# Optimization experiments

Hardware: AMD Instinct MI355X
Metric: run time of the kernel (lower is better)

The kernel has to match this reference:

```python
import jax, jax.numpy as jnp
import numpy as np

NUM_HEADS = 12
SCRA_SCALING = 10.0
EPS = 1e-12  # F.normalize default eps


def setup_inputs() -> dict:
    key = jax.random.key(0)
    ks = jax.random.split(key, 5)
    B, N, C = 2, 2048, 768
    return {
        "x": jax.random.normal(ks[0], (B, N, C), dtype=jnp.float32),
        "qkv_w": jax.random.normal(ks[1], (3 * C, C), dtype=jnp.float32) * 0.02,
        "qkv_b": jax.random.normal(ks[2], (3 * C,), dtype=jnp.float32) * 0.02,
        "proj_w": jax.random.normal(ks[3], (C, C), dtype=jnp.float32) * 0.02,
        "proj_b": jax.random.normal(ks[4], (C,), dtype=jnp.float32) * 0.02,
    }


def reference(x, qkv_w, qkv_b, proj_w, proj_b):
    B, N, C = x.shape
    H = NUM_HEADS
    D = C // H
    scale = D ** -0.5

    xt = jnp.transpose(x, (1, 0, 2))  # [N, B, C]
    qkv = xt @ qkv_w.T + qkv_b        # [N, B, 3C]
    q, k, v = jnp.split(qkv, 3, axis=-1)

    def to_bh(t):  # [N, B, C] -> [B*H, N, D]
        return jnp.transpose(t.reshape(N, B * H, D), (1, 0, 2))

    q, k, v = to_bh(q), to_bh(k), to_bh(v)

    # Stage 1: standard attention
    attn = jax.nn.softmax(jnp.einsum('bnd,bmd->bnm', q, k) * scale, axis=-1)
    out = jnp.einsum('bnm,bmd->bnd', attn, v)  # [B*H, N, D]
    out = jnp.transpose(out, (1, 0, 2)).reshape(N, B, C)
    out = out @ proj_w.T + proj_b              # first proj
    out = jnp.transpose(out.reshape(N, B * H, D), (1, 0, 2))  # [B*H, N, D]

    # Stage 2: self-correlation attention with data-dependent masking
    norm = jnp.linalg.norm(out, axis=-1, keepdims=True)
    sim_tokens = out / jnp.maximum(norm, EPS)
    sim = jnp.einsum('bnd,bmd->bnm', sim_tokens, sim_tokens) * SCRA_SCALING
    sim = jnp.where(sim < 0, -jnp.inf, sim)
    sim = jax.nn.softmax(sim, axis=-1)
    out2 = jnp.einsum('bnm,bmd->bnd', sim, v)
    out2 = jnp.transpose(out2, (1, 0, 2)).reshape(N, B, C)
    out2 = out2 @ proj_w.T + proj_b            # second proj (same weights)

    return jnp.transpose(out2, (1, 0, 2))      # [B, N, C]
```

## Files before the change

### kernel.cpp

```cpp
#include <hip/hip_runtime.h>

typedef unsigned short u16;
typedef __bf16 bf16_t;
typedef bf16_t bf16x8 __attribute__((ext_vector_type(8)));
typedef float f32x4 __attribute__((ext_vector_type(4)));

static __device__ __forceinline__ u16 f2bf(float f) {
  unsigned u = __builtin_bit_cast(unsigned, f);
  u += 0x7FFFu + ((u >> 16) & 1u);
  return (u16)(u >> 16);
}
static __device__ __forceinline__ bf16x8 ldfrag(const u16* p) {
  return __builtin_bit_cast(bf16x8, *(const uint4*)p);
}
static __device__ __forceinline__ float fexp2(float x) {
#if __has_builtin(__builtin_amdgcn_exp2f)
  return __builtin_amdgcn_exp2f(x);
#else
  return __expf(x * 0.69314718056f);
#endif
}
static __device__ __forceinline__ unsigned pack_hi16(unsigned hi, unsigned lo) {
#if __has_builtin(__builtin_amdgcn_perm)
  return __builtin_amdgcn_perm(hi, lo, 0x07060302u);
#else
  return (lo >> 16) | (hi & 0xFFFF0000u);
#endif
}
static __device__ __forceinline__ uint4 pack8_rtz(float4 a, float4 b) {
  uint4 o;
  o.x = pack_hi16(__builtin_bit_cast(unsigned, a.y), __builtin_bit_cast(unsigned, a.x));
  o.y = pack_hi16(__builtin_bit_cast(unsigned, a.w), __builtin_bit_cast(unsigned, a.z));
  o.z = pack_hi16(__builtin_bit_cast(unsigned, b.y), __builtin_bit_cast(unsigned, b.x));
  o.w = pack_hi16(__builtin_bit_cast(unsigned, b.w), __builtin_bit_cast(unsigned, b.z));
  return o;
}
static __device__ __forceinline__ int sw(int row, int chunk) {
  return (row << 6) + ((chunk ^ (row & 7)) << 3);
}

#define QWSZ 1769472
#define PWSZ 589824

__global__ __launch_bounds__(256) void convert_w(
    const float* __restrict__ qw, const float* __restrict__ pw,
    u16* __restrict__ qwb, u16* __restrict__ pwb)
{
  const int i = (blockIdx.x * 256 + threadIdx.x) * 8;
  const float* src; u16* dst; int off;
  if (i < QWSZ) { src = qw; dst = qwb; off = i; }
  else { src = pw; dst = pwb; off = i - QWSZ; }
  float4 a = *(const float4*)(src + off), b = *(const float4*)(src + off + 4);
  u16 t[8] = {f2bf(a.x), f2bf(a.y), f2bf(a.z), f2bf(a.w),
              f2bf(b.x), f2bf(b.y), f2bf(b.z), f2bf(b.w)};
  *(uint4*)(dst + off) = *(const uint4*)t;
}

template<int MODE>
__global__ __launch_bounds__(256, MODE == 0 ? 2 : 3) void gemm_nt(
    const void* __restrict__ Araw, const u16* __restrict__ W,
    const float* __restrict__ bias,
    u16* __restrict__ d0, u16* __restrict__ d1, u16* __restrict__ d2,
    float* __restrict__ df)
{
  constexpr int BM = (MODE == 0) ? 128 : 64;
  constexpr int MI = (MODE == 0) ? 4 : 2;
  constexpr int AP = BM / 32;
  __shared__ __align__(16) u16 sA[2][BM * 64];
  __shared__ __align__(16) u16 sB[2][128 * 64];
  const float* Af = (const float*)Araw;
  const u16*   Ab = (const u16*)Araw;
  const int tid = threadIdx.x;
  const int m0 = blockIdx.y * BM, n0 = blockIdx.x * 128;
  const int w = tid >> 6, lane = tid & 63, l16 = lane & 15, quad = lane >> 4;
  const int wm = (w >> 1) * (BM / 2), wn = (w & 1) * 64;

  f32x4 acc[MI][4] = {};
  const int sr = tid >> 3, ch = tid & 7, sc = ch * 8;

  #pragma unroll
  for (int p = 0; p < AP; p++) {
    const int row = sr + p * 32;
    if (MODE == 0) {
      const float* ap = Af + (size_t)(m0 + row) * 768 + sc;
      *(uint4*)(sA[0] + sw(row, ch)) =
          pack8_rtz(*(const float4*)ap, *(const float4*)(ap + 4));
    } else {
      *(uint4*)(sA[0] + sw(row, ch)) =
          *(const uint4*)(Ab + (size_t)(m0 + row) * 768 + sc);
    }
  }
  #pragma unroll
  for (int p = 0; p < 4; p++) {
    const int row = sr + p * 32;
    *(uint4*)(sB[0] + sw(row, ch)) = *(const uint4*)(W + (size_t)(n0 + row) * 768 + sc);
  }
  __syncthreads();

  for (int kt = 0; kt < 12; kt++) {
    const int buf = kt & 1;
    const bool pre = (kt + 1 < 12);
    float4 ra0[AP], ra1[AP];
    uint4 rab[AP], rb[4];
    if (pre) {
      const int kc = (kt + 1) * 64 + sc;
      #pragma unroll
      for (int p = 0; p < AP; p++) {
        if (MODE == 0) {
          const float* ap = Af + (size_t)(m0 + sr + p * 32) * 768 + kc;
          ra0[p] = *(const float4*)ap;
          ra1[p] = *(const float4*)(ap + 4);
        } else {
          rab[p] = *(const uint4*)(Ab + (size_t)(m0 + sr + p * 32) * 768 + kc);
        }
      }
      #pragma unroll
      for (int p = 0; p < 4; p++)
        rb[p] = *(const uint4*)(W + (size_t)(n0 + sr + p * 32) * 768 + kc);
    }
    #pragma unroll
    for (int ks = 0; ks < 2; ks++) {
      bf16x8 af[MI], bfv[4];
      #pragma unroll
      for (int i = 0; i < MI; i++)
        af[i] = ldfrag(sA[buf] + sw(wm + i * 16 + l16, ks * 4 + quad));
      #pragma unroll
      for (int i = 0; i < 4; i++)
        bfv[i] = ldfrag(sB[buf] + sw(wn + i * 16 + l16, ks * 4 + quad));
      #pragma unroll
      for (int mi = 0; mi < MI; mi++)
        #pragma unroll
        for (int ni = 0; ni < 4; ni++)
          acc[mi][ni] = __builtin_amdgcn_mfma_f32_16x16x32_bf16(af[mi], bfv[ni], acc[mi][ni], 0, 0, 0);
    }
    if (pre) {
      #pragma unroll
      for (int p = 0; p < AP; p++) {
        if (MODE == 0)
          *(uint4*)(sA[buf ^ 1] + sw(sr + p * 32, ch)) = pack8_rtz(ra0[p], ra1[p]);
        else
          *(uint4*)(sA[buf ^ 1] + sw(sr + p * 32, ch)) = rab[p];
      }
      #pragma unroll
      for (int p = 0; p < 4; p++)
        *(uint4*)(sB[buf ^ 1] + sw(sr + p * 32, ch)) = rb[p];
    }
    __syncthreads();
  }

  if (MODE == 0) {
    #pragma unroll
    for (int ni = 0; ni < 4; ni++) {
      const int gn = n0 + wn + ni * 16 + l16;
      const float bv = bias[gn];
      const int which = gn / 768;
      const int c = gn - which * 768, hh = c >> 6, d = c & 63;
      #pragma unroll
      for (int mi = 0; mi < 4; mi++) {
        const int gm0 = m0 + wm + mi * 16 + quad * 4;
        const int bb = gm0 >> 11, nt0 = gm0 & 2047;
        if (which == 2) {
          u16 t[4];
          #pragma unroll
          for (int r = 0; r < 4; r++) t[r] = f2bf(acc[mi][ni][r] + bv);
          *(uint2*)(d2 + (((size_t)(bb * 12 + hh)) * 64 + d) * 2048 + nt0) =
              *(const uint2*)t;
        } else {
          u16* dst = (which == 0) ? d0 : d1;
          #pragma unroll
          for (int r = 0; r < 4; r++)
            dst[(((size_t)(bb * 12 + hh)) * 2048 + nt0 + r) * 64 + d] =
                f2bf(acc[mi][ni][r] + bv);
        }
      }
    }
  } else if (MODE == 1) {
    #pragma unroll
    for (int mi = 0; mi < MI; mi++) {
      #pragma unroll
      for (int r = 0; r < 4; r++) {
        float v[4]; float ss = 0.f;
        #pragma unroll
        for (int ni = 0; ni < 4; ni++) {
          v[ni] = acc[mi][ni][r] + bias[n0 + wn + ni * 16 + l16];
          ss += v[ni] * v[ni];
        }
        #pragma unroll
        for (int off = 1; off < 16; off <<= 1) ss += __shfl_xor(ss, off);
        const float scl = 1.f / fmaxf(sqrtf(ss), 1e-12f);
        const int gm = m0 + wm + mi * 16 + quad * 4 + r;
        const int nt = gm >> 1, b = gm & 1;
        #pragma unroll
        for (int ni = 0; ni < 4; ni++) {
          const int gn = n0 + wn + ni * 16 + l16, h = gn >> 6, d = gn & 63;
          d0[(((size_t)(b * 12 + h)) * 2048 + nt) * 64 + d] = f2bf(v[ni] * scl);
        }
      }
    }
  } else {
    #pragma unroll
    for (int ni = 0; ni < 4; ni++) {
      const int gn = n0 + wn + ni * 16 + l16;
      const float bv = bias[gn];
      #pragma unroll
      for (int mi = 0; mi < MI; mi++) {
        #pragma unroll
        for (int r = 0; r < 4; r++) {
          const int gm = m0 + wm + mi * 16 + quad * 4 + r;
          const int nt = gm >> 1, b = gm & 1;
          df[((size_t)b * 2048 + nt) * 768 + gn] = acc[mi][ni][r] + bv;
        }
      }
    }
  }
}

template<int MODE>
__global__ __launch_bounds__(256, 2) void flash_attn(
    const u16* __restrict__ Qm, const u16* __restrict__ Km,
    const u16* __restrict__ VT,
    float* __restrict__ partN, float* __restrict__ partL)
{
  constexpr int N = 2048;
  __shared__ __align__(16) u16 sU[128 * 64];
  __shared__ __align__(16) u16 sK[2][64 * 64];
  __shared__ __align__(16) u16 sVT[2][64 * 64];
  const int tid = threadIdx.x;
  const int bh = blockIdx.y;
  const int qt = blockIdx.x >> 1, half = blockIdx.x & 1;
  const int m0 = qt * 128, j0 = half * 1024;
  const int w = tid >> 6, lane = tid & 63, l16 = lane & 15, quad = lane >> 4;

  constexpr float SC = (MODE == 1) ? 0.18033688011112042f
                                   : 14.426950408889634f;
  constexpr float M0 = (MODE == 1) ? 24.f : 14.6f;

  const u16* kbase = Km + (size_t)bh * N * 64;
  const u16* vbase = VT + (size_t)bh * 64 * N;
  const int qr = tid >> 1, qc = (tid & 1) * 4;
  const int sr4 = tid >> 2, c4 = tid & 3;
  {
    const u16* qp = Qm + ((size_t)bh * N + m0 + qr) * 64 + qc * 8;
    #pragma unroll
    for (int j = 0; j < 4; j++)
      *(uint4*)(sU + sw(qr, qc + j)) = *(const uint4*)(qp + j * 8);
    const u16* kp = kbase + (size_t)(j0 + sr4) * 64;
    *(uint4*)(sK[0] + sw(sr4, c4))     = *(const uint4*)(kp + c4 * 8);
    *(uint4*)(sK[0] + sw(sr4, c4 + 4)) = *(const uint4*)(kp + c4 * 8 + 32);
    const u16* vp = vbase + (size_t)sr4 * N + j0;
    *(uint4*)(sVT[0] + sw(sr4, c4))     = *(const uint4*)(vp + c4 * 8);
    *(uint4*)(sVT[0] + sw(sr4, c4 + 4)) = *(const uint4*)(vp + c4 * 8 + 32);
  }
  __syncthreads();
  bf16x8 qf[2][2];
  #pragma unroll
  for (int qg = 0; qg < 2; qg++) {
    qf[qg][0] = ldfrag(sU + sw(w * 32 + qg * 16 + l16, quad));
    qf[qg][1] = ldfrag(sU + sw(w * 32 + qg * 16 + l16, quad + 4));
  }
  asm volatile("s_waitcnt lgkmcnt(0)" ::: "memory");

  bf16x8 ones;
  #pragma unroll
  for (int i = 0; i < 8; i++) ones[i] = (bf16_t)1.0f;

  f32x4 oacc[2][4] = {};
  f32x4 lacc[2] = {};

  for (int it = 0; it < 16; it++) {
    const int buf = it & 1;
    const u16* sKb = sK[buf];
    const u16* sVb = sVT[buf];
    u16* sKn = sK[buf ^ 1];
    u16* sVn = sVT[buf ^ 1];

    uint4 pk0, pk1, pv0, pv1;
    const bool pre = (it + 1 < 16);
    if (pre) {
      const int j1 = j0 + (it + 1) * 64;
      const u16* kp = kbase + (size_t)(j1 + sr4) * 64;
      pk0 = *(const uint4*)(kp + c4 * 8);
      pk1 = *(const uint4*)(kp + c4 * 8 + 32);
      const u16* vp = vbase + (size_t)sr4 * N + j1;
      pv0 = *(const uint4*)(vp + c4 * 8);
      pv1 = *(const uint4*)(vp + c4 * 8 + 32);
    }

    f32x4 s[2][4];
    #pragma unroll
    for (int jt = 0; jt < 4; jt++) {
      bf16x8 kf0 = ldfrag(sKb + sw(jt * 16 + l16, quad));
      bf16x8 kf1 = ldfrag(sKb + sw(jt * 16 + l16, quad + 4));
      #pragma unroll
      for (int qg = 0; qg < 2; qg++) {
        f32x4 a = {};
        a = __builtin_amdgcn_mfma_f32_16x16x32_bf16(kf0, qf[qg][0], a, 0, 0, 0);
        a = __builtin_amdgcn_mfma_f32_16x16x32_bf16(kf1, qf[qg][1], a, 0, 0, 0);
        s[qg][jt] = a;
      }
    }

    #pragma unroll
    for (int qg = 0; qg < 2; qg++) {
      const int prow = w * 32 + qg * 16 + l16;
      #pragma unroll
      for (int jt = 0; jt < 4; jt++) {
        unsigned pu[4];
        #pragma unroll
        for (int r = 0; r < 4; r++) {
          const float a = s[qg][jt][r];
          float p = fexp2(fmaf(a, SC, -M0));
          if (MODE == 2 && a < 0.f) p = 0.f;
          pu[r] = __builtin_bit_cast(unsigned, p) & 0xFFFF0000u;
        }
        uint2 pkk;
        pkk.x = pack_hi16(pu[1], pu[0]);
        pkk.y = pack_hi16(pu[3], pu[2]);
        *(uint2*)(sU + sw(prow, 2 * jt + (quad >> 1)) + (quad & 1) * 4) = pkk;
      }
    }

    asm volatile("s_waitcnt lgkmcnt(0)" ::: "memory");
    bf16x8 pf[2][2];
    #pragma unroll
    for (int qg = 0; qg < 2; qg++) {
      pf[qg][0] = ldfrag(sU + sw(w * 32 + qg * 16 + l16, quad));
      pf[qg][1] = ldfrag(sU + sw(w * 32 + qg * 16 + l16, quad + 4));
    }

    if (pre) {
      *(uint4*)(sKn + sw(sr4, c4))     = pk0;
      *(uint4*)(sKn + sw(sr4, c4 + 4)) = pk1;
      *(uint4*)(sVn + sw(sr4, c4))     = pv0;
      *(uint4*)(sVn + sw(sr4, c4 + 4)) = pv1;
    }

    #pragma unroll
    for (int d4 = 0; d4 < 4; d4++) {
      bf16x8 v0 = ldfrag(sVb + sw(d4 * 16 + l16, quad));
      bf16x8 v1 = ldfrag(sVb + sw(d4 * 16 + l16, quad + 4));
      #pragma unroll
      for (int qg = 0; qg < 2; qg++) {
        oacc[qg][d4] = __builtin_amdgcn_mfma_f32_16x16x32_bf16(v0, pf[qg][0], oacc[qg][d4], 0, 0, 0);
        oacc[qg][d4] = __builtin_amdgcn_mfma_f32_16x16x32_bf16(v1, pf[qg][1], oacc[qg][d4], 0, 0, 0);
      }
    }
    #pragma unroll
    for (int qg = 0; qg < 2; qg++) {
      lacc[qg] = __builtin_amdgcn_mfma_f32_16x16x32_bf16(ones, pf[qg][0], lacc[qg], 0, 0, 0);
      lacc[qg] = __builtin_amdgcn_mfma_f32_16x16x32_bf16(ones, pf[qg][1], lacc[qg], 0, 0, 0);
    }
    __syncthreads();
  }

  const int blk = bh * 32 + blockIdx.x;
  float* pN = partN + (size_t)blk * 8192 + tid * 32;
  #pragma unroll
  for (int qg = 0; qg < 2; qg++) {
    #pragma unroll
    for (int d4 = 0; d4 < 4; d4++)
      *(f32x4*)(pN + qg * 16 + d4 * 4) = oacc[qg][d4];
    if (quad == 0)
      partL[blk * 128 + w * 32 + qg * 16 + l16] = lacc[qg][0];
  }
}

__global__ __launch_bounds__(256) void combine_flash(
    const float* __restrict__ partN, const float* __restrict__ partL,
    u16* __restrict__ Ob)
{
  const int pair = blockIdx.x;
  const int bh = pair >> 4, qt = pair & 15;
  const int b = bh / 12, h = bh % 12;
  const int m0 = qt * 128;
  const int tid = threadIdx.x;
  const int w = tid >> 6, lane = tid & 63, l16 = lane & 15, quad = lane >> 4;
  const int blk0 = bh * 32 + qt * 2, blk1 = blk0 + 1;
  const float* n0 = partN + (size_t)blk0 * 8192 + tid * 32;
  const float* n1 = partN + (size_t)blk1 * 8192 + tid * 32;
  #pragma unroll
  for (int qg = 0; qg < 2; qg++) {
    const int qrow = w * 32 + qg * 16 + l16;
    const float l0 = partL[blk0 * 128 + qrow];
    const float l1 = partL[blk1 * 128 + qrow];
    const float inv = 1.f / fmaxf(l0 + l1, 1e-30f);
    const int query = m0 + qrow;
    u16* obase = Ob + ((size_t)query * 2 + b) * 768 + h * 64;
    #pragma unroll
    for (int d4 = 0; d4 < 4; d4++) {
      float4 a = *(const float4*)(n0 + qg * 16 + d4 * 4);
      float4 c = *(const float4*)(n1 + qg * 16 + d4 * 4);
      u16 t[4] = {f2bf((a.x + c.x) * inv), f2bf((a.y + c.y) * inv),
                  f2bf((a.z + c.z) * inv), f2bf((a.w + c.w) * inv)};
      *(uint2*)(obase + d4 * 16 + quad * 4) = *(const uint2*)t;
    }
  }
}

extern "C" void kernel_launch(void* const* d_in, const int* in_sizes, int n_in,
                              void* d_out, int out_size, void* d_ws, size_t ws_size,
                              hipStream_t stream) {
  const float* x      = (const float*)d_in[0];
  const float* qkv_w  = (const float*)d_in[1];
  const float* qkv_b  = (const float*)d_in[2];
  const float* proj_w = (const float*)d_in[3];
  const float* proj_b = (const float*)d_in[4];
  float* out = (float*)d_out;

  const size_t SZ = (size_t)24 * 2048 * 64;
  char* ws = (char*)d_ws;
  u16* vtb = (u16*)ws;
  size_t off = SZ * 2;
  u16* qwb = (u16*)(ws + off); off += (size_t)QWSZ * 2;
  u16* pwb = (u16*)(ws + off); off += (size_t)PWSZ * 2;
  u16* qb  = (u16*)(ws + off); off += SZ * 2;
  u16* kb  = (u16*)(ws + off); off += SZ * 2;
  float* partN = (float*)(ws + off); off += (size_t)768 * 8192 * 4;
  float* partL = (float*)(ws + off); off += (size_t)768 * 128 * 4;
  u16* o1 = qb;
  u16* o2 = qb;
  u16* st = kb;

  convert_w<<<1152, 256, 0, stream>>>(qkv_w, proj_w, qwb, pwb);
  gemm_nt<0><<<dim3(18, 32), 256, 0, stream>>>(x, qwb, qkv_b, qb, kb, vtb, nullptr);
  flash_attn<1><<<dim3(32, 24), 256, 0, stream>>>(qb, kb, vtb, partN, partL);
  combine_flash<<<384, 256, 0, stream>>>(partN, partL, o1);
  gemm_nt<1><<<dim3(6, 64), 256, 0, stream>>>(o1, pwb, proj_b, st, nullptr, nullptr, nullptr);
  flash_attn<2><<<dim3(32, 24), 256, 0, stream>>>(st, st, vtb, partN, partL);
  combine_flash<<<384, 256, 0, stream>>>(partN, partL, o2);
  gemm_nt<2><<<dim3(6, 64), 256, 0, stream>>>(o2, pwb, proj_b, nullptr, nullptr, nullptr, out);
}
```

Baseline: 240.3 us.

## Pre-convert x to bf16, shrink QKV GEMM tiles, single-buffer flash K/V

Folds the fp32-to-bf16 conversion of x into the weight-conversion kernel, storing it in the partN workspace, so the QKV GEMM reads bf16 input. The QKV GEMM now uses 64-row tiles with a larger grid and higher occupancy hint. The flash attention kernel drops double-buffered K/V shared memory for a single buffer, adding an extra barrier before writing prefetched tiles. This cuts LDS use to allow more blocks per CU, at the cost of less overlap and an extra pass over x.

```diff
diff --git a/kernel.cpp b/kernel.cpp
--- a/kernel.cpp
+++ b/kernel.cpp
@@ -27,29 +27,24 @@
   return (lo >> 16) | (hi & 0xFFFF0000u);
 #endif
 }
-static __device__ __forceinline__ uint4 pack8_rtz(float4 a, float4 b) {
-  uint4 o;
-  o.x = pack_hi16(__builtin_bit_cast(unsigned, a.y), __builtin_bit_cast(unsigned, a.x));
-  o.y = pack_hi16(__builtin_bit_cast(unsigned, a.w), __builtin_bit_cast(unsigned, a.z));
-  o.z = pack_hi16(__builtin_bit_cast(unsigned, b.y), __builtin_bit_cast(unsigned, b.x));
-  o.w = pack_hi16(__builtin_bit_cast(unsigned, b.w), __builtin_bit_cast(unsigned, b.z));
-  return o;
-}
 static __device__ __forceinline__ int sw(int row, int chunk) {
   return (row << 6) + ((chunk ^ (row & 7)) << 3);
 }
 
+#define XSZ 3145728
 #define QWSZ 1769472
 #define PWSZ 589824
 
-__global__ __launch_bounds__(256) void convert_w(
-    const float* __restrict__ qw, const float* __restrict__ pw,
+__global__ __launch_bounds__(256) void convert_all(
+    const float* __restrict__ x, const float* __restrict__ qw,
+    const float* __restrict__ pw, u16* __restrict__ xb,
     u16* __restrict__ qwb, u16* __restrict__ pwb)
 {
   const int i = (blockIdx.x * 256 + threadIdx.x) * 8;
   const float* src; u16* dst; int off;
-  if (i < QWSZ) { src = qw; dst = qwb; off = i; }
-  else { src = pw; dst = pwb; off = i - QWSZ; }
+  if (i < XSZ) { src = x; dst = xb; off = i; }
+  else if (i < XSZ + QWSZ) { src = qw; dst = qwb; off = i - XSZ; }
+  else { src = pw; dst = pwb; off = i - (XSZ + QWSZ); }
   float4 a = *(const float4*)(src + off), b = *(const float4*)(src + off + 4);
   u16 t[8] = {f2bf(a.x), f2bf(a.y), f2bf(a.z), f2bf(a.w),
               f2bf(b.x), f2bf(b.y), f2bf(b.z), f2bf(b.w)};
@@ -57,90 +52,64 @@
 }
 
 template<int MODE>
-__global__ __launch_bounds__(256, MODE == 0 ? 2 : 3) void gemm_nt(
-    const void* __restrict__ Araw, const u16* __restrict__ W,
+__global__ __launch_bounds__(256, 3) void gemm_nt(
+    const u16* __restrict__ A, const u16* __restrict__ W,
     const float* __restrict__ bias,
     u16* __restrict__ d0, u16* __restrict__ d1, u16* __restrict__ d2,
     float* __restrict__ df)
 {
-  constexpr int BM = (MODE == 0) ? 128 : 64;
-  constexpr int MI = (MODE == 0) ? 4 : 2;
-  constexpr int AP = BM / 32;
-  __shared__ __align__(16) u16 sA[2][BM * 64];
+  __shared__ __align__(16) u16 sA[2][64 * 64];
   __shared__ __align__(16) u16 sB[2][128 * 64];
-  const float* Af = (const float*)Araw;
-  const u16*   Ab = (const u16*)Araw;
   const int tid = threadIdx.x;
-  const int m0 = blockIdx.y * BM, n0 = blockIdx.x * 128;
+  const int m0 = blockIdx.y * 64, n0 = blockIdx.x * 128;
   const int w = tid >> 6, lane = tid & 63, l16 = lane & 15, quad = lane >> 4;
-  const int wm = (w >> 1) * (BM / 2), wn = (w & 1) * 64;
-
-  f32x4 acc[MI][4] = {};
+  const int wm = (w >> 1) * 32, wn = (w & 1) * 64;
+
+  f32x4 acc[2][4] = {};
   const int sr = tid >> 3, ch = tid & 7, sc = ch * 8;
 
   #pragma unroll
-  for (int p = 0; p < AP; p++) {
-    const int row = sr + p * 32;
-    if (MODE == 0) {
-      const float* ap = Af + (size_t)(m0 + row) * 768 + sc;
-      *(uint4*)(sA[0] + sw(row, ch)) =
-          pack8_rtz(*(const float4*)ap, *(const float4*)(ap + 4));
-    } else {
-      *(uint4*)(sA[0] + sw(row, ch)) =
-          *(const uint4*)(Ab + (size_t)(m0 + row) * 768 + sc);
-    }
-  }
-  #pragma unroll
-  for (int p = 0; p < 4; p++) {
-    const int row = sr + p * 32;
-    *(uint4*)(sB[0] + sw(row, ch)) = *(const uint4*)(W + (size_t)(n0 + row) * 768 + sc);
-  }
+  for (int p = 0; p < 2; p++)
+    *(uint4*)(sA[0] + sw(sr + p * 32, ch)) =
+        *(const uint4*)(A + (size_t)(m0 + sr + p * 32) * 768 + sc);
+  #pragma unroll
+  for (int p = 0; p < 4; p++)
+    *(uint4*)(sB[0] + sw(sr + p * 32, ch)) =
+        *(const uint4*)(W + (size_t)(n0 + sr + p * 32) * 768 + sc);
   __syncthreads();
 
   for (int kt = 0; kt < 12; kt++) {
     const int buf = kt & 1;
     const bool pre = (kt + 1 < 12);
-    float4 ra0[AP], ra1[AP];
-    uint4 rab[AP], rb[4];
+    uint4 rab[2], rb[4];
     if (pre) {
       const int kc = (kt + 1) * 64 + sc;
       #pragma unroll
-      for (int p = 0; p < AP; p++) {
-        if (MODE == 0) {
-          const float* ap = Af + (size_t)(m0 + sr + p * 32) * 768 + kc;
-          ra0[p] = *(const float4*)ap;
-          ra1[p] = *(const float4*)(ap + 4);
-        } else {
-          rab[p] = *(const uint4*)(Ab + (size_t)(m0 + sr + p * 32) * 768 + kc);
-        }
-      }
+      for (int p = 0; p < 2; p++)
+        rab[p] = *(const uint4*)(A + (size_t)(m0 + sr + p * 32) * 768 + kc);
       #pragma unroll
       for (int p = 0; p < 4; p++)
         rb[p] = *(const uint4*)(W + (size_t)(n0 + sr + p * 32) * 768 + kc);
     }
     #pragma unroll
     for (int ks = 0; ks < 2; ks++) {
-      bf16x8 af[MI], bfv[4];
-      #pragma unroll
-      for (int i = 0; i < MI; i++)
+      bf16x8 af[2], bfv[4];
+      #pragma unroll
+      for (int i = 0; i < 2; i++)
         af[i] = ldfrag(sA[buf] + sw(wm + i * 16 + l16, ks * 4 + quad));
       #pragma unroll
       for (int i = 0; i < 4; i++)
         bfv[i] = ldfrag(sB[buf] + sw(wn + i * 16 + l16, ks * 4 + quad));
       #pragma unroll
-      for (int mi = 0; mi < MI; mi++)
+      for (int mi = 0; mi < 2; mi++)
         #pragma unroll
         for (int ni = 0; ni < 4; ni++)
           acc[mi][ni] = __builtin_amdgcn_mfma_f32_16x16x32_bf16(af[mi], bfv[ni], acc[mi][ni], 0, 0, 0);
     }
     if (pre) {
       #pragma unroll
-      for (int p = 0; p < AP; p++) {
-        if (MODE == 0)
-          *(uint4*)(sA[buf ^ 1] + sw(sr + p * 32, ch)) = pack8_rtz(ra0[p], ra1[p]);
-        else
-          *(uint4*)(sA[buf ^ 1] + sw(sr + p * 32, ch)) = rab[p];
-      }
+      for (int p = 0; p < 2; p++)
+        *(uint4*)(sA[buf ^ 1] + sw(sr + p * 32, ch)) = rab[p];
       #pragma unroll
       for (int p = 0; p < 4; p++)
         *(uint4*)(sB[buf ^ 1] + sw(sr + p * 32, ch)) = rb[p];
@@ -156,7 +125,7 @@
       const int which = gn / 768;
       const int c = gn - which * 768, hh = c >> 6, d = c & 63;
       #pragma unroll
-      for (int mi = 0; mi < 4; mi++) {
+      for (int mi = 0; mi < 2; mi++) {
         const int gm0 = m0 + wm + mi * 16 + quad * 4;
         const int bb = gm0 >> 11, nt0 = gm0 & 2047;
         if (which == 2) {
@@ -176,7 +145,7 @@
     }
   } else if (MODE == 1) {
     #pragma unroll
-    for (int mi = 0; mi < MI; mi++) {
+    for (int mi = 0; mi < 2; mi++) {
       #pragma unroll
       for (int r = 0; r < 4; r++) {
         float v[4]; float ss = 0.f;
@@ -203,7 +172,7 @@
       const int gn = n0 + wn + ni * 16 + l16;
       const float bv = bias[gn];
       #pragma unroll
-      for (int mi = 0; mi < MI; mi++) {
+      for (int mi = 0; mi < 2; mi++) {
         #pragma unroll
         for (int r = 0; r < 4; r++) {
           const int gm = m0 + wm + mi * 16 + quad * 4 + r;
@@ -223,8 +192,8 @@
 {
   constexpr int N = 2048;
   __shared__ __align__(16) u16 sU[128 * 64];
-  __shared__ __align__(16) u16 sK[2][64 * 64];
-  __shared__ __align__(16) u16 sVT[2][64 * 64];
+  __shared__ __align__(16) u16 sK[64 * 64];
+  __shared__ __align__(16) u16 sVT[64 * 64];
   const int tid = threadIdx.x;
   const int bh = blockIdx.y;
   const int qt = blockIdx.x >> 1, half = blockIdx.x & 1;
@@ -245,11 +214,11 @@
     for (int j = 0; j < 4; j++)
       *(uint4*)(sU + sw(qr, qc + j)) = *(const uint4*)(qp + j * 8);
     const u16* kp = kbase + (size_t)(j0 + sr4) * 64;
-    *(uint4*)(sK[0] + sw(sr4, c4))     = *(const uint4*)(kp + c4 * 8);
-    *(uint4*)(sK[0] + sw(sr4, c4 + 4)) = *(const uint4*)(kp + c4 * 8 + 32);
+    *(uint4*)(sK + sw(sr4, c4))     = *(const uint4*)(kp + c4 * 8);
+    *(uint4*)(sK + sw(sr4, c4 + 4)) = *(const uint4*)(kp + c4 * 8 + 32);
     const u16* vp = vbase + (size_t)sr4 * N + j0;
-    *(uint4*)(sVT[0] + sw(sr4, c4))     = *(const uint4*)(vp + c4 * 8);
-    *(uint4*)(sVT[0] + sw(sr4, c4 + 4)) = *(const uint4*)(vp + c4 * 8 + 32);
+    *(uint4*)(sVT + sw(sr4, c4))     = *(const uint4*)(vp + c4 * 8);
+    *(uint4*)(sVT + sw(sr4, c4 + 4)) = *(const uint4*)(vp + c4 * 8 + 32);
   }
   __syncthreads();
   bf16x8 qf[2][2];
@@ -268,12 +237,6 @@
   f32x4 lacc[2] = {};
 
   for (int it = 0; it < 16; it++) {
-    const int buf = it & 1;
-    const u16* sKb = sK[buf];
-    const u16* sVb = sVT[buf];
-    u16* sKn = sK[buf ^ 1];
-    u16* sVn = sVT[buf ^ 1];
-
     uint4 pk0, pk1, pv0, pv1;
     const bool pre = (it + 1 < 16);
     if (pre) {
@@ -289,8 +252,8 @@
     f32x4 s[2][4];
     #pragma unroll
     for (int jt = 0; jt < 4; jt++) {
-      bf16x8 kf0 = ldfrag(sKb + sw(jt * 16 + l16, quad));
-      bf16x8 kf1 = ldfrag(sKb + sw(jt * 16 + l16, quad + 4));
+      bf16x8 kf0 = ldfrag(sK + sw(jt * 16 + l16, quad));
+      bf16x8 kf1 = ldfrag(sK + sw(jt * 16 + l16, quad + 4));
       #pragma unroll
       for (int qg = 0; qg < 2; qg++) {
         f32x4 a = {};
@@ -328,17 +291,10 @@
       pf[qg][1] = ldfrag(sU + sw(w * 32 + qg * 16 + l16, quad + 4));
     }
 
-    if (pre) {
-      *(uint4*)(sKn + sw(sr4, c4))     = pk0;
-      *(uint4*)(sKn + sw(sr4, c4 + 4)) = pk1;
-      *(uint4*)(sVn + sw(sr4, c4))     = pv0;
-      *(uint4*)(sVn + sw(sr4, c4 + 4)) = pv1;
-    }
-
     #pragma unroll
     for (int d4 = 0; d4 < 4; d4++) {
-      bf16x8 v0 = ldfrag(sVb + sw(d4 * 16 + l16, quad));
-      bf16x8 v1 = ldfrag(sVb + sw(d4 * 16 + l16, quad + 4));
+      bf16x8 v0 = ldfrag(sVT + sw(d4 * 16 + l16, quad));
+      bf16x8 v1 = ldfrag(sVT + sw(d4 * 16 + l16, quad + 4));
       #pragma unroll
       for (int qg = 0; qg < 2; qg++) {
         oacc[qg][d4] = __builtin_amdgcn_mfma_f32_16x16x32_bf16(v0, pf[qg][0], oacc[qg][d4], 0, 0, 0);
@@ -349,6 +305,14 @@
     for (int qg = 0; qg < 2; qg++) {
       lacc[qg] = __builtin_amdgcn_mfma_f32_16x16x32_bf16(ones, pf[qg][0], lacc[qg], 0, 0, 0);
       lacc[qg] = __builtin_amdgcn_mfma_f32_16x16x32_bf16(ones, pf[qg][1], lacc[qg], 0, 0, 0);
+    }
+
+    __syncthreads();
+    if (pre) {
+      *(uint4*)(sK + sw(sr4, c4))      = pk0;
+      *(uint4*)(sK + sw(sr4, c4 + 4))  = pk1;
+      *(uint4*)(sVT + sw(sr4, c4))     = pv0;
+      *(uint4*)(sVT + sw(sr4, c4 + 4)) = pv1;
     }
     __syncthreads();
   }
@@ -417,12 +381,13 @@
   u16* kb  = (u16*)(ws + off); off += SZ * 2;
   float* partN = (float*)(ws + off); off += (size_t)768 * 8192 * 4;
   float* partL = (float*)(ws + off); off += (size_t)768 * 128 * 4;
+  u16* xb = (u16*)partN;
   u16* o1 = qb;
   u16* o2 = qb;
   u16* st = kb;
 
-  convert_w<<<1152, 256, 0, stream>>>(qkv_w, proj_w, qwb, pwb);
-  gemm_nt<0><<<dim3(18, 32), 256, 0, stream>>>(x, qwb, qkv_b, qb, kb, vtb, nullptr);
+  convert_all<<<2688, 256, 0, stream>>>(x, qkv_w, proj_w, xb, qwb, pwb);
+  gemm_nt<0><<<dim3(18, 64), 256, 0, stream>>>(xb, qwb, qkv_b, qb, kb, vtb, nullptr);
   flash_attn<1><<<dim3(32, 24), 256, 0, stream>>>(qb, kb, vtb, partN, partL);
   combine_flash<<<384, 256, 0, stream>>>(partN, partL, o1);
   gemm_nt<1><<<dim3(6, 64), 256, 0, stream>>>(o1, pwb, proj_b, st, nullptr, nullptr, nullptr);
```

Result: faster. 231.9 us (-3.5%).
